# Kernel optimization log

Measured on AMD Instinct MI355X. Metric: run time of the kernel, lower is better.

The kernel has to match this reference:

```python
import jax, jax.numpy as jnp
import numpy as np
import math

ESM_DIM = 1280

def setup_inputs() -> dict:
    key = jax.random.key(0)
    ks = jax.random.split(key, 12)
    B, Ls, Lc, D = 16, 1024, 2048, ESM_DIM
    scale = 0.02
    return {
        "cyclase": jax.random.normal(ks[0], (B, Lc, D), jnp.float32),
        "substrate": jax.random.normal(ks[1], (B, Ls, D), jnp.float32),
        "cyclase_mask": jnp.ones((B, Lc), jnp.float32),
        "substrate_mask": jnp.ones((B, Ls), jnp.float32),
        "Wq": jax.random.uniform(ks[2], (D, D), jnp.float32) * scale,
        "Wk": jax.random.uniform(ks[3], (D, D), jnp.float32) * scale,
        "Wv": jax.random.uniform(ks[4], (D, D), jnp.float32) * scale,
        "W1": jax.random.normal(ks[5], (2 * D, 512), jnp.float32) * scale,
        "b1": jnp.zeros((512,), jnp.float32),
        "W2": jax.random.normal(ks[6], (512, 64), jnp.float32) * scale,
        "b2": jnp.zeros((64,), jnp.float32),
        "W3": jax.random.normal(ks[7], (64, 1), jnp.float32) * scale,
        "b3": jnp.zeros((1,), jnp.float32),
    }


def reference(cyclase, substrate, cyclase_mask, substrate_mask,
              Wq, Wk, Wv, W1, b1, W2, b2, W3, b3):
    # Cross attention: substrate is the query, cyclase is key/value.
    q = jnp.einsum('bsd,de->bse', substrate, Wq)   # [B,Ls,D]
    k = jnp.einsum('bcd,de->bce', cyclase, Wk)     # [B,Lc,D]
    v = jnp.einsum('bcd,de->bce', cyclase, Wv)     # [B,Lc,D]
    scores = jnp.einsum('bse,bce->bsc', q, k) / math.sqrt(q.shape[-1])
    # NOTE: original torch code masks `attn_scores` but softmaxes
    # `scaled_attn_scores`, so the padding mask has no effect. Replicated.
    weights = jax.nn.softmax(scores, axis=-1)      # [B,Ls,Lc]
    attn_out = jnp.einsum('bsc,bce->bse', weights, v)  # [B,Ls,D]
    x1_avg = jnp.mean(attn_out, axis=1)            # [B,D]
    sub_avg = jnp.mean(substrate, axis=1)          # [B,D]
    x = jnp.concatenate([x1_avg, sub_avg], axis=1) # [B,2D]
    h = jax.nn.relu(x @ W1 + b1)
    h = jax.nn.relu(h @ W2 + b2)
    return jax.nn.sigmoid(h @ W3 + b3)             # [B,1]
```

## Files before the change

kernel.cpp:

```cpp
#include <hip/hip_runtime.h>
#include <hip/hip_bf16.h>

#define DEV static __device__ __forceinline__

typedef __attribute__((ext_vector_type(16))) float f32x16;
typedef __attribute__((ext_vector_type(8)))  short bf16x8;

#if defined(__has_builtin)
#  if __has_builtin(__builtin_amdgcn_cvt_pk_fp8_f32) && __has_builtin(__builtin_amdgcn_cvt_f32_fp8)
#    define HW_FP8 1
#  endif
#endif

DEV ushort f2bf(float f){
  union { float f; unsigned u; } v; v.f = f;
  return (ushort)((v.u + 0x7FFFu + ((v.u >> 16) & 1u)) >> 16);
}
DEV float bf2f(ushort u){
  union { unsigned u; float f; } v; v.u = ((unsigned)u) << 16;
  return v.f;
}

DEV unsigned char f2e4m3_sw(float f){
  union { float f; unsigned u; } v; v.f = f;
  unsigned s = (v.u >> 24) & 0x80;
  float a = fabsf(f);
  if (a >= 448.f) return s | 0x7E;
  if (a < 0.0009765625f) return (unsigned char)s;
  if (a < 0.015625f) {
    int m = (int)rintf(a * 512.f);
    return (unsigned char)(s | (m >= 8 ? 8 : m));
  }
  unsigned ab = v.u & 0x7FFFFFFF;
  unsigned r = ab + 0x0007FFFF + ((ab >> 20) & 1);
  unsigned e = (r >> 23) - 127 + 7;
  unsigned m = (r >> 20) & 7;
  if (e > 15 || (e == 15 && m > 6)) return s | 0x7E;
  return (unsigned char)(s | (e << 3) | m);
}
DEV float e4m32f_sw(unsigned char c){
  unsigned e = (c >> 3) & 15, m = c & 7;
  float v;
  if (e) { union { unsigned u; float f; } w; w.u = ((e + 120u) << 23) | (m << 20); v = w.f; }
  else v = (float)m * 0.001953125f;
  return (c & 0x80) ? -v : v;
}

DEV unsigned pack4_fp8(float a, float b, float c, float d){
#ifdef HW_FP8
  int v = __builtin_amdgcn_cvt_pk_fp8_f32(a, b, 0, false);
  v = __builtin_amdgcn_cvt_pk_fp8_f32(c, d, v, true);
  return (unsigned)v;
#else
  return (unsigned)f2e4m3_sw(a) | ((unsigned)f2e4m3_sw(b) << 8)
       | ((unsigned)f2e4m3_sw(c) << 16) | ((unsigned)f2e4m3_sw(d) << 24);
#endif
}
DEV unsigned char enc_fp8(float a){
#ifdef HW_FP8
  return (unsigned char)(__builtin_amdgcn_cvt_pk_fp8_f32(a, a, 0, false) & 0xFF);
#else
  return f2e4m3_sw(a);
#endif
}
template<int SEL>
DEV float dec_fp8(unsigned u){
#ifdef HW_FP8
  return __builtin_amdgcn_cvt_f32_fp8((int)u, SEL);
#else
  return e4m32f_sw((u >> (SEL * 8)) & 0xFF);
#endif
}

DEV void gload16(const void* g, void* l) {
  __builtin_amdgcn_global_load_lds(
      (const __attribute__((address_space(1))) unsigned*)g,
      (__attribute__((address_space(3))) unsigned*)l, 16, 0, 0);
}

__global__ __launch_bounds__(256)
void cvt_bf16(const float* __restrict__ src, ushort* __restrict__ dst, long n8)
{
  const long stride = (long)gridDim.x * 256;
  for (long i = (long)blockIdx.x * 256 + threadIdx.x; i < n8; i += stride) {
    const float4 a = *(const float4*)(src + i * 8);
    const float4 b = *(const float4*)(src + i * 8 + 4);
    union { ushort u[8]; uint4 v; } pk;
    pk.u[0] = f2bf(a.x); pk.u[1] = f2bf(a.y); pk.u[2] = f2bf(a.z); pk.u[3] = f2bf(a.w);
    pk.u[4] = f2bf(b.x); pk.u[5] = f2bf(b.y); pk.u[6] = f2bf(b.z); pk.u[7] = f2bf(b.w);
    *(uint4*)(dst + i * 8) = pk.v;
  }
}

__global__ __launch_bounds__(256)
void cyccvt(const float* __restrict__ cyc, unsigned* __restrict__ cyc8w,
            float* __restrict__ gsum)
{
  const int lane = threadIdx.x & 63, wid = threadIdx.x >> 6;
  const long row = (long)blockIdx.x * 4 + wid;
  const float* src = cyc + row * 1280;
  unsigned* dst = cyc8w + row * 320;
  float s = 0.f;
  #pragma unroll
  for (int i = 0; i < 5; i++) {
    const int d = i * 256 + lane * 4;
    const float4 v = *(const float4*)(src + d);
    s += v.x + v.y + v.z + v.w;
    dst[d >> 2] = pack4_fp8(v.x * 16.f, v.y * 16.f, v.z * 16.f, v.w * 16.f);
  }
  #pragma unroll
  for (int o = 1; o < 64; o <<= 1) s += __shfl_xor(s, o);
  if (lane == 0) gsum[row] = s;
}

__global__ __launch_bounds__(256)
void subprep(const float* __restrict__ sub, const float* __restrict__ mcol,
             unsigned* __restrict__ sub8w, float* __restrict__ tbar)
{
  __shared__ float mc[1280];
  for (int i = threadIdx.x; i < 1280; i += 256) mc[i] = mcol[i];
  __syncthreads();
  const int lane = threadIdx.x & 63, wid = threadIdx.x >> 6;
  const long row = (long)blockIdx.x * 4 + wid;
  const float4* sp = (const float4*)(sub + row * 1280);
  unsigned* dp = sub8w + row * 320;
  float d = 0.f;
  #pragma unroll
  for (int i = 0; i < 5; i++) {
    const int c = i * 64 + lane;
    const float4 v = sp[c];
    d += v.x * mc[c * 4] + v.y * mc[c * 4 + 1] + v.z * mc[c * 4 + 2] + v.w * mc[c * 4 + 3];
    dp[c] = pack4_fp8(v.x * 16.f, v.y * 16.f, v.z * 16.f, v.w * 16.f);
  }
  #pragma unroll
  for (int o = 1; o < 64; o <<= 1) d += __shfl_xor(d, o);
  if (lane == 0) tbar[row] = d;
}

__global__ __launch_bounds__(512, 4)
void gemm_mkq(const ushort* __restrict__ A, const ushort* __restrict__ B,
              ushort* __restrict__ C, int K, int N, int nbx, float scale)
{
  __shared__ __align__(16) ushort As[4][4][128][8];
  __shared__ __align__(16) ushort Bs[4][4][128][8];
  const int tid = threadIdx.x, lane = tid & 63, wid = tid >> 6;
  const int wr = wid >> 2, wc = wid & 3;
  const int bx = blockIdx.x % nbx, by = blockIdx.x / nbx;
  const int bm = by * 128, bn = bx * 128;

  f32x16 acc[2];
  #pragma unroll
  for (int i = 0; i < 2; i++)
    #pragma unroll
    for (int e = 0; e < 16; e++) acc[i][e] = 0.f;

  const int kbA = wid >> 1, rqA = wid & 1;
  const ushort* agp = A + (long)(bm + rqA * 64 + lane) * K + kbA * 8;
  const ushort* bgp = B + (long)(bn + rqA * 64 + lane) * K + kbA * 8;
  auto STAGE = [&](int g, int rg) {
    gload16(agp + g * 32, &As[rg][kbA][rqA * 64][0]);
    gload16(bgp + g * 32, &Bs[rg][kbA][rqA * 64][0]);
  };
  const int NG = K >> 5;
  STAGE(0, 0); STAGE(1, 1);
  asm volatile("s_waitcnt vmcnt(2)" ::: "memory");
  __builtin_amdgcn_s_barrier();
  const int lkh = lane >> 5, lr = lane & 31;
  auto GROUP = [&](int g, int rg, int rg2) {
    bf16x8 av[2][2], bv[2];
    #pragma unroll
    for (int kf = 0; kf < 2; kf++) {
      #pragma unroll
      for (int mi = 0; mi < 2; mi++)
        av[mi][kf] = *(const bf16x8*)&As[rg][kf * 2 + lkh][wr * 64 + mi * 32 + lr][0];
      bv[kf] = *(const bf16x8*)&Bs[rg][kf * 2 + lkh][wc * 32 + lr][0];
    }
    if (g + 2 < NG) STAGE(g + 2, rg2);
    __builtin_amdgcn_s_barrier();
    __builtin_amdgcn_s_setprio(1);
    #pragma unroll
    for (int mi = 0; mi < 2; mi++)
      #pragma unroll
      for (int kf = 0; kf < 2; kf++)
        acc[mi] = __builtin_amdgcn_mfma_f32_32x32x16_bf16(av[mi][kf], bv[kf], acc[mi], 0, 0, 0);
    __builtin_amdgcn_s_setprio(0);
    if (g + 2 < NG)      asm volatile("s_waitcnt vmcnt(2)" ::: "memory");
    else if (g + 1 < NG) asm volatile("s_waitcnt vmcnt(0)" ::: "memory");
    __builtin_amdgcn_s_barrier();
  };
  for (int g = 0; g < NG; g += 4) {
    GROUP(g, 0, 2); GROUP(g + 1, 1, 3); GROUP(g + 2, 2, 0); GROUP(g + 3, 3, 1);
  }
  #pragma unroll
  for (int mi = 0; mi < 2; mi++)
    #pragma unroll
    for (int rr = 0; rr < 16; rr++) {
      const int row = bm + wr * 64 + mi * 32 + (rr & 3) + 8 * (rr >> 2) + 4 * lkh;
      const int col = bn + wc * 32 + lr;
      C[(long)row * N + col] = f2bf(acc[mi][rr] * scale);
    }
}

__global__ __launch_bounds__(256)
void colmean(const ushort* __restrict__ Mkq, float* __restrict__ mcol)
{
  const int d = blockIdx.x * 256 + threadIdx.x;
  const int r0 = blockIdx.y * 40;
  float s = 0.f;
  for (int j = 0; j < 40; j++) s += bf2f(Mkq[(long)(r0 + j) * 1280 + d]);
  atomicAdd(&mcol[d], s * (1.f / 1280.f));
}

__global__ __launch_bounds__(320)
void m2cvt(const ushort* __restrict__ Mkq, const float* __restrict__ mcol,
           unsigned* __restrict__ M2w)
{
  const int j = blockIdx.x;
  const int d = threadIdx.x * 4;
  const ushort* mr = Mkq + (long)j * 1280 + d;
  const float* mc = mcol + d;
  M2w[j * 320 + threadIdx.x] = pack4_fp8(
      (bf2f(mr[0]) - mc[0]) * 524288.f, (bf2f(mr[1]) - mc[1]) * 524288.f,
      (bf2f(mr[2]) - mc[2]) * 524288.f, (bf2f(mr[3]) - mc[3]) * 524288.f);
}

template<int MODE, bool BY_FAST>
__global__ __launch_bounds__(512, 2)
void gemm_f8(const unsigned char* __restrict__ A, const unsigned char* __restrict__ B,
             void* __restrict__ Cv, int K, int N, int nbx, int nby,
             long sA, long sB, long sC,
             const float* __restrict__ tbar, const float* __restrict__ gsum)
{
  __shared__ __align__(16) unsigned char As[4][4][256][16];
  __shared__ __align__(16) unsigned char Bs[4][4][256][16];
  const int tid = threadIdx.x, lane = tid & 63, wid = tid >> 6;
  const int wr = wid >> 2, wc = wid & 3;

  const int nwg = gridDim.x;
  const int q = nwg >> 3, r = nwg & 7;
  const int xcd = blockIdx.x & 7, lid = blockIdx.x >> 3;
  const int id = (xcd < r ? xcd * (q + 1) : r * (q + 1) + (xcd - r) * q) + lid;
  const int per = nbx * nby;
  const int z = id / per, rem = id - z * per;
  const int bx = BY_FAST ? rem / nby : rem % nbx;
  const int by = BY_FAST ? rem % nby : rem / nbx;
  const int bm = by * 256, bn = bx * 256;
  const long Ab = (long)z * sA, Bb = (long)z * sB, Cb = (long)z * sC;

  f32x16 acc[4][2];
  #pragma unroll
  for (int i = 0; i < 4; i++)
    #pragma unroll
    for (int j = 0; j < 2; j++)
      #pragma unroll
      for (int e = 0; e < 16; e++) acc[i][j][e] = 0.f;

  const int c0 = wid * 2, c1 = wid * 2 + 1;
  const int kb0 = c0 >> 2, rq0 = c0 & 3, kb1 = c1 >> 2, rq1 = c1 & 3;
  const unsigned char* ag0 = A + Ab + (long)(bm + rq0 * 64 + lane) * K + kb0 * 16;
  const unsigned char* ag1 = A + Ab + (long)(bm + rq1 * 64 + lane) * K + kb1 * 16;
  const unsigned char* bg0 = B + Bb + (long)(bn + rq0 * 64 + lane) * K + kb0 * 16;
  const unsigned char* bg1 = B + Bb + (long)(bn + rq1 * 64 + lane) * K + kb1 * 16;
  auto STAGE_A = [&](int g, int rg) {
    gload16(ag0 + g * 64, &As[rg][kb0][rq0 * 64][0]);
    gload16(ag1 + g * 64, &As[rg][kb1][rq1 * 64][0]);
  };
  auto STAGE_B = [&](int g, int rg) {
    gload16(bg0 + g * 64, &Bs[rg][kb0][rq0 * 64][0]);
    gload16(bg1 + g * 64, &Bs[rg][kb1][rq1 * 64][0]);
  };

  const int NG = K >> 6;
  STAGE_A(0, 0); STAGE_B(0, 0); STAGE_A(1, 1); STAGE_B(1, 1);
  asm volatile("s_waitcnt vmcnt(4)" ::: "memory");
  __builtin_amdgcn_s_barrier();

  const int lkh = lane >> 5, lr = lane & 31;

  auto GROUP = [&](int g, int rg, int rg2) {
    const bool pre = (g + 2 < NG);
    long av[2][4], bv[2][4];
    #pragma unroll
    for (int kf = 0; kf < 4; kf++) {
      #pragma unroll
      for (int mi = 0; mi < 2; mi++)
        av[mi][kf] = *(const long*)&As[rg][kf][wr * 128 + mi * 32 + lr][lkh * 8];
      #pragma unroll
      for (int ni = 0; ni < 2; ni++)
        bv[ni][kf] = *(const long*)&Bs[rg][kf][wc * 64 + ni * 32 + lr][lkh * 8];
    }
    if (pre) STAGE_A(g + 2, rg2);
    __builtin_amdgcn_s_barrier();
    __builtin_amdgcn_s_setprio(1);
    #pragma unroll
    for (int kf = 0; kf < 4; kf++)
      #pragma unroll
      for (int mi = 0; mi < 2; mi++)
        #pragma unroll
        for (int ni = 0; ni < 2; ni++)
          acc[mi][ni] = __builtin_amdgcn_mfma_f32_32x32x16_fp8_fp8(av[mi][kf], bv[ni][kf], acc[mi][ni], 0, 0, 0);
    __builtin_amdgcn_s_setprio(0);
    __builtin_amdgcn_s_barrier();
    #pragma unroll
    for (int kf = 0; kf < 4; kf++)
      #pragma unroll
      for (int mi = 0; mi < 2; mi++)
        av[mi][kf] = *(const long*)&As[rg][kf][wr * 128 + (mi + 2) * 32 + lr][lkh * 8];
    if (pre) STAGE_B(g + 2, rg2);
    __builtin_amdgcn_s_barrier();
    __builtin_amdgcn_s_setprio(1);
    #pragma unroll
    for (int kf = 0; kf < 4; kf++)
      #pragma unroll
      for (int mi = 0; mi < 2; mi++)
        #pragma unroll
        for (int ni = 0; ni < 2; ni++)
          acc[mi + 2][ni] = __builtin_amdgcn_mfma_f32_32x32x16_fp8_fp8(av[mi][kf], bv[ni][kf], acc[mi + 2][ni], 0, 0, 0);
    __builtin_amdgcn_s_setprio(0);
    if (pre)             asm volatile("s_waitcnt vmcnt(4)" ::: "memory");
    else if (g + 1 < NG) asm volatile("s_waitcnt vmcnt(0)" ::: "memory");
    __builtin_amdgcn_s_barrier();
  };

  for (int g = 0; g < NG; g += 4) {
    GROUP(g, 0, 2); GROUP(g + 1, 1, 3); GROUP(g + 2, 2, 0); GROUP(g + 3, 3, 1);
  }

  #pragma unroll
  for (int mi = 0; mi < 4; mi++)
    #pragma unroll
    for (int ni = 0; ni < 2; ni++)
      #pragma unroll
      for (int rr = 0; rr < 16; rr++) {
        const int row = bm + wr * 128 + mi * 32 + (rr & 3) + 8 * (rr >> 2) + 4 * lkh;
        const int col = bn + wc * 64 + ni * 32 + lr;
        if constexpr (MODE == 0) {
          const float v = acc[mi][ni][rr] * 0x1p-16f
                        + tbar[(long)z * 1024 + row] * gsum[(long)z * 2048 + col];
          ((ushort*)Cv)[Cb + (long)row * N + col] = f2bf(v);
        } else {
          ((unsigned char*)Cv)[Cb + (long)row * N + col] = enc_fp8(acc[mi][ni][rr] * 0x1p-11f);
        }
      }
}

__global__ __launch_bounds__(512, 4)
void gemm_f8_128(const unsigned char* __restrict__ A, const unsigned char* __restrict__ B,
                 unsigned char* __restrict__ C, int K, int N, int nbx)
{
  __shared__ __align__(16) unsigned char As[4][4][128][16];
  __shared__ __align__(16) unsigned char Bs[4][4][128][16];
  const int tid = threadIdx.x, lane = tid & 63, wid = tid >> 6;
  const int wr = wid >> 2, wc = wid & 3;

  const int nwg = gridDim.x;
  const int q = nwg >> 3, r = nwg & 7;
  const int xcd = blockIdx.x & 7, lid = blockIdx.x >> 3;
  const int id = (xcd < r ? xcd * (q + 1) : r * (q + 1) + (xcd - r) * q) + lid;
  const int bx = id % nbx, by = id / nbx;
  const int bm = by * 128, bn = bx * 128;

  f32x16 acc[2];
  #pragma unroll
  for (int i = 0; i < 2; i++)
    #pragma unroll
    for (int e = 0; e < 16; e++) acc[i][e] = 0.f;

  const int kbA = wid >> 1, rhA = wid & 1;
  const unsigned char* agp = A + (long)(bm + rhA * 64 + lane) * K + kbA * 16;
  const unsigned char* bgp = B + (long)(bn + rhA * 64 + lane) * K + kbA * 16;
  auto STAGE = [&](int g, int rg) {
    gload16(agp + g * 64, &As[rg][kbA][rhA * 64][0]);
    gload16(bgp + g * 64, &Bs[rg][kbA][rhA * 64][0]);
  };
  const int NG = K >> 6;
  STAGE(0, 0); STAGE(1, 1);
  asm volatile("s_waitcnt vmcnt(2)" ::: "memory");
  __builtin_amdgcn_s_barrier();

  const int lkh = lane >> 5, lr = lane & 31;

  auto GROUP = [&](int g, int rg, int rg2) {
    long av[2][4], bv[4];
    #pragma unroll
    for (int kf = 0; kf < 4; kf++) {
      #pragma unroll
      for (int mi = 0; mi < 2; mi++)
        av[mi][kf] = *(const long*)&As[rg][kf][wr * 64 + mi * 32 + lr][lkh * 8];
      bv[kf] = *(const long*)&Bs[rg][kf][wc * 32 + lr][lkh * 8];
    }
    if (g + 2 < NG) STAGE(g + 2, rg2);
    __builtin_amdgcn_s_barrier();
    __builtin_amdgcn_s_setprio(1);
    #pragma unroll
    for (int kf = 0; kf < 4; kf++)
      #pragma unroll
      for (int mi = 0; mi < 2; mi++)
        acc[mi] = __builtin_amdgcn_mfma_f32_32x32x16_fp8_fp8(av[mi][kf], bv[kf], acc[mi], 0, 0, 0);
    __builtin_amdgcn_s_setprio(0);
    if (g + 2 < NG)      asm volatile("s_waitcnt vmcnt(2)" ::: "memory");
    else if (g + 1 < NG) asm volatile("s_waitcnt vmcnt(0)" ::: "memory");
    __builtin_amdgcn_s_barrier();
  };
  for (int g = 0; g < NG; g += 4) {
    GROUP(g, 0, 2); GROUP(g + 1, 1, 3); GROUP(g + 2, 2, 0); GROUP(g + 3, 3, 1);
  }

  #pragma unroll
  for (int mi = 0; mi < 2; mi++)
    #pragma unroll
    for (int rr = 0; rr < 16; rr++) {
      const int row = bm + wr * 64 + mi * 32 + (rr & 3) + 8 * (rr >> 2) + 4 * lkh;
      const int col = bn + wc * 32 + lr;
      C[(long)row * N + col] = enc_fp8(acc[mi][rr] * 0x1p-11f);
    }
}

__global__ __launch_bounds__(256)
void softmax_wsum(const ushort* __restrict__ S, float* __restrict__ wsum)
{
  const int b = blockIdx.x;
  const int s0 = blockIdx.y * 32;
  const int lane = threadIdx.x & 63;
  const int w = threadIdx.x >> 6;
  __shared__ float red[4][2048];
  const ushort* Sb = S + (((long)b * 1024) + s0 + w * 8) * 2048;

  float acc[32];
  #pragma unroll
  for (int i = 0; i < 32; i++) acc[i] = 0.f;
  for (int r = 0; r < 8; r++) {
    const ushort* row = Sb + (long)r * 2048;
    float v[32];
    #pragma unroll
    for (int i = 0; i < 4; i++) {
      uint4 u = *(const uint4*)(row + i * 512 + lane * 8);
      const ushort* up = (const ushort*)&u;
      #pragma unroll
      for (int j = 0; j < 8; j++) v[i * 8 + j] = bf2f(up[j]);
    }
    float m = v[0];
    #pragma unroll
    for (int i = 1; i < 32; i++) m = fmaxf(m, v[i]);
    #pragma unroll
    for (int o = 1; o < 64; o <<= 1) m = fmaxf(m, __shfl_xor(m, o));
    float ssum = 0.f;
    #pragma unroll
    for (int i = 0; i < 32; i++) { v[i] = __expf(v[i] - m); ssum += v[i]; }
    #pragma unroll
    for (int o = 1; o < 64; o <<= 1) ssum += __shfl_xor(ssum, o);
    const float inv = 1.f / ssum;
    #pragma unroll
    for (int i = 0; i < 32; i++) acc[i] += v[i] * inv;
  }
  #pragma unroll
  for (int i = 0; i < 4; i++)
    #pragma unroll
    for (int j = 0; j < 8; j++)
      red[w][i * 512 + lane * 8 + j] = acc[i * 8 + j];
  __syncthreads();
  float* wb = wsum + b * 2048;
  #pragma unroll
  for (int k = 0; k < 8; k++) {
    const int c = k * 256 + threadIdx.x;
    atomicAdd(&wb[c], red[0][c] + red[1][c] + red[2][c] + red[3][c]);
  }
}

__global__ __launch_bounds__(320)
void wcyc_kernel(const unsigned char* __restrict__ cyc8, const float* __restrict__ wsum,
                 float* __restrict__ t)
{
  const int b = blockIdx.x;
  const int c0 = blockIdx.y * 64;
  const int d = threadIdx.x * 4;
  const unsigned char* cb = cyc8 + ((long)b * 2048 + c0) * 1280 + d;
  const float* wb = wsum + b * 2048 + c0;
  float4 a = {0.f, 0.f, 0.f, 0.f};
  for (int c = 0; c < 64; c++) {
    const unsigned u = *(const unsigned*)(cb + (long)c * 1280);
    const float w = wb[c];
    a.x += w * dec_fp8<0>(u); a.y += w * dec_fp8<1>(u);
    a.z += w * dec_fp8<2>(u); a.w += w * dec_fp8<3>(u);
  }
  atomicAdd(&t[b * 1280 + d + 0], a.x * 0.0625f);
  atomicAdd(&t[b * 1280 + d + 1], a.y * 0.0625f);
  atomicAdd(&t[b * 1280 + d + 2], a.z * 0.0625f);
  atomicAdd(&t[b * 1280 + d + 3], a.w * 0.0625f);
}

__global__ __launch_bounds__(320)
void submean8(const unsigned char* __restrict__ sub8, float* __restrict__ xcat)
{
  const int b = blockIdx.x;
  const int s0 = blockIdx.y * 64;
  const int d = threadIdx.x * 4;
  const unsigned char* sp = sub8 + ((long)b * 1024 + s0) * 1280 + d;
  float4 a = {0.f, 0.f, 0.f, 0.f};
  for (int s = 0; s < 64; s++) {
    const unsigned u = *(const unsigned*)(sp + (long)s * 1280);
    a.x += dec_fp8<0>(u); a.y += dec_fp8<1>(u);
    a.z += dec_fp8<2>(u); a.w += dec_fp8<3>(u);
  }
  const float k = 1.f / (16.f * 1024.f);
  atomicAdd(&xcat[b * 2560 + 1280 + d + 0], a.x * k);
  atomicAdd(&xcat[b * 2560 + 1280 + d + 1], a.y * k);
  atomicAdd(&xcat[b * 2560 + 1280 + d + 2], a.z * k);
  atomicAdd(&xcat[b * 2560 + 1280 + d + 3], a.w * k);
}

__global__ __launch_bounds__(256)
void xv_fused(const float* __restrict__ t, const float* __restrict__ Wv,
              float* __restrict__ xcat)
{
  const int dp0 = blockIdx.x * 64;
  const int d0 = blockIdx.y * 256;
  __shared__ float tl[16 * 256];
  __shared__ float red[4][64][16];
  for (int i = threadIdx.x; i < 16 * 256; i += 256) {
    const int b = i >> 8, d = i & 255;
    tl[i] = t[b * 1280 + d0 + d];
  }
  __syncthreads();
  const int dpi = threadIdx.x & 63;
  const int grp = threadIdx.x >> 6;
  float acc[16];
  #pragma unroll
  for (int b = 0; b < 16; b++) acc[b] = 0.f;
  for (int dd = 0; dd < 64; dd++) {
    const int d = grp * 64 + dd;
    const float w = Wv[(long)(d0 + d) * 1280 + dp0 + dpi];
    #pragma unroll
    for (int b = 0; b < 16; b++) acc[b] += w * tl[b * 256 + d];
  }
  #pragma unroll
  for (int b = 0; b < 16; b++) red[grp][dpi][b] = acc[b];
  __syncthreads();
  #pragma unroll
  for (int k = 0; k < 4; k++) {
    const int o = k * 256 + threadIdx.x;
    const int dp = o >> 4, b = o & 15;
    const float v = red[0][dp][b] + red[1][dp][b] + red[2][dp][b] + red[3][dp][b];
    atomicAdd(&xcat[b * 2560 + dp0 + dp], v * (1.f / 1024.f));
  }
}

__global__ __launch_bounds__(256)
void mlp1_fused(const float* __restrict__ xcat, const float* __restrict__ W1,
                float* __restrict__ h1pre)
{
  const int j0 = blockIdx.x * 64;
  const int d0 = blockIdx.y * 320;
  __shared__ float xl[16 * 320];
  __shared__ float red[4][64][16];
  for (int i = threadIdx.x; i < 16 * 320; i += 256) {
    const int b = i / 320, d = i % 320;
    xl[i] = xcat[b * 2560 + d0 + d];
  }
  __syncthreads();
  const int ji = threadIdx.x & 63;
  const int grp = threadIdx.x >> 6;
  float acc[16];
  #pragma unroll
  for (int b = 0; b < 16; b++) acc[b] = 0.f;
  for (int dd = 0; dd < 80; dd++) {
    const int d = grp * 80 + dd;
    const float w = W1[(long)(d0 + d) * 512 + j0 + ji];
    #pragma unroll
    for (int b = 0; b < 16; b++) acc[b] += w * xl[b * 320 + d];
  }
  #pragma unroll
  for (int b = 0; b < 16; b++) red[grp][ji][b] = acc[b];
  __syncthreads();
  #pragma unroll
  for (int k = 0; k < 4; k++) {
    const int o = k * 256 + threadIdx.x;
    const int j = o >> 4, b = o & 15;
    const float v = red[0][j][b] + red[1][j][b] + red[2][j][b] + red[3][j][b];
    atomicAdd(&h1pre[b * 512 + j0 + j], v);
  }
}

__global__ __launch_bounds__(64)
void mlp23_kernel(const float* __restrict__ h1pre, const float* __restrict__ b1,
                  const float* __restrict__ W2, const float* __restrict__ b2,
                  const float* __restrict__ W3, const float* __restrict__ b3,
                  float* __restrict__ out)
{
  const int b = blockIdx.x;
  const int j = threadIdx.x;
  __shared__ float hl[512];
  for (int i = j; i < 512; i += 64) hl[i] = fmaxf(h1pre[b * 512 + i] + b1[i], 0.f);
  __syncthreads();
  float a = b2[j];
  for (int d = 0; d < 512; d++) a += hl[d] * W2[d * 64 + j];
  a = fmaxf(a, 0.f);
  float p = a * W3[j];
  #pragma unroll
  for (int o = 1; o < 64; o <<= 1) p += __shfl_xor(p, o);
  if (j == 0) out[b] = 1.f / (1.f + __expf(-(p + b3[0])));
}

extern "C" void kernel_launch(void* const* d_in, const int* in_sizes, int n_in,
                              void* d_out, int out_size, void* d_ws, size_t ws_size,
                              hipStream_t stream)
{
  const float* cyclase   = (const float*)d_in[0];
  const float* substrate = (const float*)d_in[1];
  const float* Wq = (const float*)d_in[4];
  const float* Wk = (const float*)d_in[5];
  const float* Wv = (const float*)d_in[6];
  const float* W1 = (const float*)d_in[7];
  const float* b1 = (const float*)d_in[8];
  const float* W2 = (const float*)d_in[9];
  const float* b2 = (const float*)d_in[10];
  const float* W3 = (const float*)d_in[11];
  const float* b3 = (const float*)d_in[12];
  float* out = (float*)d_out;
  (void)in_sizes; (void)n_in; (void)out_size; (void)ws_size;

  char* ws = (char*)d_ws;
  unsigned char* cyc8 = (unsigned char*)ws;
  char* A2 = ws + 41943040;
  ushort* Mkq   = (ushort*)(A2 + 41943040);
  ushort* Wq16  = (ushort*)(A2 + 41943040 + 3276800);
  ushort* Wk16  = (ushort*)(A2 + 41943040 + 2 * 3276800);
  unsigned char* sub8 = (unsigned char*)(A2 + 41943040 + 3 * 3276800);
  ushort* S = (ushort*)A2;
  char* B2 = A2 + 41943040 + 3 * 3276800 + 20971520;
  unsigned char* T1p8 = (unsigned char*)B2;
  unsigned char* M2_8 = (unsigned char*)(B2 + 20971520);
  char* C2 = B2 + 20971520 + 1638400;
  float* mcol  = (float*)C2;
  float* tbar  = (float*)(C2 + 8192);
  float* gsum  = (float*)(C2 + 8192 + 65536);
  float* wsum  = (float*)(C2 + 8192 + 65536 + 131072);
  float* tbuf  = (float*)(C2 + 8192 + 65536 + 2 * 131072);
  float* xcat  = (float*)(C2 + 8192 + 65536 + 2 * 131072 + 81920);
  float* h1pre = (float*)(C2 + 8192 + 65536 + 2 * 131072 + 81920 + 163840);

  hipMemsetAsync(mcol, 0, 1280 * 4, stream);
  hipMemsetAsync(wsum, 0, 16 * 2048 * 4, stream);
  hipMemsetAsync(tbuf, 0, 16 * 1280 * 4, stream);
  hipMemsetAsync(xcat, 0, 16 * 2560 * 4, stream);
  hipMemsetAsync(h1pre, 0, 16 * 512 * 4, stream);

  cvt_bf16<<<200, 256, 0, stream>>>(Wq, Wq16, 1280l * 1280 / 8);
  cvt_bf16<<<200, 256, 0, stream>>>(Wk, Wk16, 1280l * 1280 / 8);
  cyccvt<<<8192, 256, 0, stream>>>(cyclase, (unsigned*)cyc8, gsum);

  gemm_mkq<<<100, 512, 0, stream>>>(Wk16, Wq16, Mkq, 1280, 1280, 10,
                                    0.02795084971874737f);
  colmean<<<dim3(5, 32), 256, 0, stream>>>(Mkq, mcol);
  m2cvt<<<1280, 320, 0, stream>>>(Mkq, mcol, (unsigned*)M2_8);

  subprep<<<4096, 256, 0, stream>>>(substrate, mcol, (unsigned*)sub8, tbar);
  submean8<<<dim3(16, 16), 320, 0, stream>>>(sub8, xcat);

  gemm_f8_128<<<1280, 512, 0, stream>>>(sub8, M2_8, T1p8, 1280, 1280, 10);

  gemm_f8<0, true><<<512, 512, 0, stream>>>(T1p8, cyc8, S,
      1280, 2048, 8, 4, 1024l * 1280, 2048l * 1280, 1024l * 2048, tbar, gsum);

  softmax_wsum<<<dim3(16, 32), 256, 0, stream>>>(S, wsum);
  wcyc_kernel<<<dim3(16, 32), 320, 0, stream>>>(cyc8, wsum, tbuf);
  xv_fused<<<dim3(20, 5), 256, 0, stream>>>(tbuf, Wv, xcat);
  mlp1_fused<<<dim3(8, 8), 256, 0, stream>>>(xcat, W1, h1pre);
  mlp23_kernel<<<16, 64, 0, stream>>>(h1pre, b1, W2, b2, W3, b3, out);
}
```

Baseline: 380.3 us.

## Merge launches, fold column mean into GEMM epilogue, split softmax rows finer

```diff
diff --git a/kernel.cpp b/kernel.cpp
--- a/kernel.cpp
+++ b/kernel.cpp
@@ -79,8 +79,12 @@
 }
 
 __global__ __launch_bounds__(256)
-void cvt_bf16(const float* __restrict__ src, ushort* __restrict__ dst, long n8)
-{
+void cvt_wqk(const float* __restrict__ Wq, const float* __restrict__ Wk,
+             ushort* __restrict__ Wq16, ushort* __restrict__ Wk16)
+{
+  const float* src = blockIdx.y ? Wk : Wq;
+  ushort* dst = blockIdx.y ? Wk16 : Wq16;
+  const long n8 = 1280l * 1280 / 8;
   const long stride = (long)gridDim.x * 256;
   for (long i = (long)blockIdx.x * 256 + threadIdx.x; i < n8; i += stride) {
     const float4 a = *(const float4*)(src + i * 8);
@@ -139,7 +143,8 @@
 
 __global__ __launch_bounds__(512, 4)
 void gemm_mkq(const ushort* __restrict__ A, const ushort* __restrict__ B,
-              ushort* __restrict__ C, int K, int N, int nbx, float scale)
+              ushort* __restrict__ C, int K, int N, int nbx, float scale,
+              float* __restrict__ mcol)
 {
   __shared__ __align__(16) ushort As[4][4][128][8];
   __shared__ __align__(16) ushort Bs[4][4][128][8];
@@ -191,24 +196,18 @@
   for (int g = 0; g < NG; g += 4) {
     GROUP(g, 0, 2); GROUP(g + 1, 1, 3); GROUP(g + 2, 2, 0); GROUP(g + 3, 3, 1);
   }
+  float csum = 0.f;
   #pragma unroll
   for (int mi = 0; mi < 2; mi++)
     #pragma unroll
     for (int rr = 0; rr < 16; rr++) {
       const int row = bm + wr * 64 + mi * 32 + (rr & 3) + 8 * (rr >> 2) + 4 * lkh;
       const int col = bn + wc * 32 + lr;
-      C[(long)row * N + col] = f2bf(acc[mi][rr] * scale);
+      const float v = acc[mi][rr] * scale;
+      csum += v;
+      C[(long)row * N + col] = f2bf(v);
     }
-}
-
-__global__ __launch_bounds__(256)
-void colmean(const ushort* __restrict__ Mkq, float* __restrict__ mcol)
-{
-  const int d = blockIdx.x * 256 + threadIdx.x;
-  const int r0 = blockIdx.y * 40;
-  float s = 0.f;
-  for (int j = 0; j < 40; j++) s += bf2f(Mkq[(long)(r0 + j) * 1280 + d]);
-  atomicAdd(&mcol[d], s * (1.f / 1280.f));
+  atomicAdd(&mcol[bn + wc * 32 + lr], csum * (1.f / 1280.f));
 }
 
 __global__ __launch_bounds__(320)
@@ -420,16 +419,16 @@
 void softmax_wsum(const ushort* __restrict__ S, float* __restrict__ wsum)
 {
   const int b = blockIdx.x;
-  const int s0 = blockIdx.y * 32;
+  const int s0 = blockIdx.y * 16;
   const int lane = threadIdx.x & 63;
   const int w = threadIdx.x >> 6;
   __shared__ float red[4][2048];
-  const ushort* Sb = S + (((long)b * 1024) + s0 + w * 8) * 2048;
+  const ushort* Sb = S + (((long)b * 1024) + s0 + w * 4) * 2048;
 
   float acc[32];
   #pragma unroll
   for (int i = 0; i < 32; i++) acc[i] = 0.f;
-  for (int r = 0; r < 8; r++) {
+  for (int r = 0; r < 4; r++) {
     const ushort* row = Sb + (long)r * 2048;
     float v[32];
     #pragma unroll
@@ -639,19 +638,13 @@
   float* xcat  = (float*)(C2 + 8192 + 65536 + 2 * 131072 + 81920);
   float* h1pre = (float*)(C2 + 8192 + 65536 + 2 * 131072 + 81920 + 163840);
 
-  hipMemsetAsync(mcol, 0, 1280 * 4, stream);
-  hipMemsetAsync(wsum, 0, 16 * 2048 * 4, stream);
-  hipMemsetAsync(tbuf, 0, 16 * 1280 * 4, stream);
-  hipMemsetAsync(xcat, 0, 16 * 2560 * 4, stream);
-  hipMemsetAsync(h1pre, 0, 16 * 512 * 4, stream);
-
-  cvt_bf16<<<200, 256, 0, stream>>>(Wq, Wq16, 1280l * 1280 / 8);
-  cvt_bf16<<<200, 256, 0, stream>>>(Wk, Wk16, 1280l * 1280 / 8);
+  hipMemsetAsync(C2, 0, 8192 + 65536 + 2 * 131072 + 81920 + 163840 + 32768, stream);
+
+  cvt_wqk<<<dim3(200, 2), 256, 0, stream>>>(Wq, Wk, Wq16, Wk16);
   cyccvt<<<8192, 256, 0, stream>>>(cyclase, (unsigned*)cyc8, gsum);
 
   gemm_mkq<<<100, 512, 0, stream>>>(Wk16, Wq16, Mkq, 1280, 1280, 10,
-                                    0.02795084971874737f);
-  colmean<<<dim3(5, 32), 256, 0, stream>>>(Mkq, mcol);
+                                    0.02795084971874737f, mcol);
   m2cvt<<<1280, 320, 0, stream>>>(Mkq, mcol, (unsigned*)M2_8);
 
   subprep<<<4096, 256, 0, stream>>>(substrate, mcol, (unsigned*)sub8, tbar);
@@ -662,7 +655,7 @@
   gemm_f8<0, true><<<512, 512, 0, stream>>>(T1p8, cyc8, S,
       1280, 2048, 8, 4, 1024l * 1280, 2048l * 1280, 1024l * 2048, tbar, gsum);
 
-  softmax_wsum<<<dim3(16, 32), 256, 0, stream>>>(S, wsum);
+  softmax_wsum<<<dim3(16, 64), 256, 0, stream>>>(S, wsum);
   wcyc_kernel<<<dim3(16, 32), 320, 0, stream>>>(cyc8, wsum, tbuf);
   xv_fused<<<dim3(20, 5), 256, 0, stream>>>(tbuf, Wv, xcat);
   mlp1_fused<<<dim3(8, 8), 256, 0, stream>>>(xcat, W1, h1pre);
```

New measurement: 368.2 us, median of 2. -3.2%, faster.
